# Performance work log

Measured on AMD Instinct MI355X. Metric: run time of the kernel, lower is better.

The kernel has to match this reference:

```python
import jax, jax.numpy as jnp
import numpy as np

# Model dims (from DecoderLSTM defaults)
H = 512       # hidden_size
E = 128       # embedding_dim == input_size
NC = 27       # num_class (output_size)
NE = 28       # num_embeddings = num_class + 1
B = 256       # batch
T = 512       # timesteps


def setup_inputs() -> dict:
    key = jax.random.key(0)
    ks = jax.random.split(key, 12)
    s = 0.05
    return {
        "target_inputs": jax.random.randint(ks[0], (B, T), 0, NE),
        "target_lengths": jax.random.randint(ks[1], (B,), 1, T + 1),
        "h0": jax.random.normal(ks[2], (4, B, H), dtype=jnp.float32),   # [num_layer*num_dirs, B, H]
        "c0": jax.random.normal(ks[3], (4, B, H), dtype=jnp.float32),
        "embed": jax.random.normal(ks[4], (NE, E), dtype=jnp.float32) * s,
        "Wih0": jax.random.normal(ks[5], (2, 4 * H, E), dtype=jnp.float32) * s,      # layer0 [dir,4H,E]
        "Wih1": jax.random.normal(ks[6], (2, 4 * H, 2 * H), dtype=jnp.float32) * s,  # layer1 [dir,4H,2H]
        "Whh": jax.random.normal(ks[7], (2, 2, 4 * H, H), dtype=jnp.float32) * s,    # [layer,dir,4H,H]
        "bih": jax.random.normal(ks[8], (2, 2, 4 * H), dtype=jnp.float32) * s,
        "bhh": jax.random.normal(ks[9], (2, 2, 4 * H), dtype=jnp.float32) * s,
        "Wout": jax.random.normal(ks[10], (NC, 2 * H), dtype=jnp.float32) * s,
        "bout": jax.random.normal(ks[11], (NC,), dtype=jnp.float32) * s,
    }


def _lstm_cell(x, h, c, Wih, Whh, b):
    # x: [B,in], h/c: [B,H]; PyTorch gate order i,f,g,o
    g = x @ Wih.T + h @ Whh.T + b
    i, f, gg, o = jnp.split(g, 4, axis=-1)
    c2 = jax.nn.sigmoid(f) * c + jax.nn.sigmoid(i) * jnp.tanh(gg)
    h2 = jax.nn.sigmoid(o) * jnp.tanh(c2)
    return h2, c2


def reference(target_inputs, target_lengths, h0, c0, embed,
              Wih0, Wih1, Whh, bih, bhh, Wout, bout):
    b = bih + bhh                              # [layer,dir,4H]
    x_emb = embed[target_inputs]               # [B,T,E]
    seq_len = target_inputs.shape[1]

    def step(carry, xt):
        h, c = carry                           # [4,B,H] each; layout layer*2+dir
        hf, cf = _lstm_cell(xt, h[0], c[0], Wih0[0], Whh[0, 0], b[0, 0])
        hb, cb = _lstm_cell(xt, h[1], c[1], Wih0[1], Whh[0, 1], b[0, 1])
        y0 = jnp.concatenate([hf, hb], axis=-1)                 # [B,2H]
        h2f, c2f = _lstm_cell(y0, h[2], c[2], Wih1[0], Whh[1, 0], b[1, 0])
        h2b, c2b = _lstm_cell(y0, h[3], c[3], Wih1[1], Whh[1, 1], b[1, 1])
        y1 = jnp.concatenate([h2f, h2b], axis=-1)               # [B,2H]
        hn = jnp.stack([hf, hb, h2f, h2b])
        cn = jnp.stack([cf, cb, c2f, c2b])
        return (hn, cn), y1 @ Wout.T + bout                      # logits [B,NC]

    _, logits_t = jax.lax.scan(step, (h0, c0), jnp.swapaxes(x_emb, 0, 1))
    logits = jnp.swapaxes(logits_t, 0, 1)                        # [B,T,NC]
    mask = jnp.arange(seq_len)[None, :] < target_lengths[:, None]
    outputs = jnp.where(mask[:, :, None], logits, jnp.zeros((), logits.dtype))
    return outputs, target_lengths
```

## Files before the change

kernel.cpp:

```cpp
#include <hip/hip_runtime.h>
#include <hip/hip_bf16.h>
#include <stdint.h>

typedef unsigned short ushort_t;
typedef unsigned char u8_t;
typedef unsigned long long u64_t;

#define H   512
#define E   128
#define NC  27
#define NE  28
#define B   256
#define T   512
#define FH  2048
#define NPH (T + 2)
#define NL0 64
#define NL1 128
#define NOUT 32
#define BHs (B * H)
#define WOFF_L0 131072
#define WOFF_L1 65536
#define LDS_BYTES (160 * 1024)
#define CROW 256

typedef __bf16 bf16x8 __attribute__((ext_vector_type(8)));
typedef float  f32x4  __attribute__((ext_vector_type(4)));

#define WAITV(n) asm volatile("s_waitcnt vmcnt(" #n ")" ::: "memory")
#define LADDER8(rem) do { if ((rem) >= 7) WAITV(7); else if ((rem) == 6) WAITV(6); \
                          else if ((rem) == 5) WAITV(5); else if ((rem) == 4) WAITV(4); \
                          else if ((rem) == 3) WAITV(3); else if ((rem) == 2) WAITV(2); \
                          else if ((rem) == 1) WAITV(1); else WAITV(0); } while (0)

__device__ __forceinline__ ushort_t f2b(float x) {
    uint32_t u = __float_as_uint(x);
    uint32_t r = (u + 0x7FFFu + ((u >> 16) & 1u)) >> 16;
    return (ushort_t)r;
}
__device__ __forceinline__ u8_t f2fp8(float x) {
    uint32_t u = __float_as_uint(x);
    uint32_t s = (u >> 24) & 0x80u;
    int E8 = (int)((u >> 23) & 0xffu);
    uint32_t M = u & 0x7fffffu;
    if (E8 == 0) return (u8_t)s;
    int e8 = E8 - 120;
    uint32_t code;
    if (e8 <= 0) {
        int sh = 1 - e8;
        if (sh > 23) return (u8_t)s;
        code = (0x800000u | M) >> sh;
    } else {
        code = ((uint32_t)e8 << 23) | M;
    }
    uint32_t r = (code + 0x7ffffu + ((code >> 20) & 1u)) >> 20;
    if (r > 0x7eu) r = 0x7eu;
    return (u8_t)(s | r);
}
__device__ __forceinline__ float sigm(float x) {
    return 1.f / (1.f + __expf(-x));
}
__device__ __forceinline__ void stc1(u8_t* p, u8_t v) {
    __hip_atomic_store(p, v, __ATOMIC_RELAXED, __HIP_MEMORY_SCOPE_AGENT);
}
__device__ __forceinline__ void stc2(ushort_t* p, ushort_t v) {
    __hip_atomic_store(p, v, __ATOMIC_RELAXED, __HIP_MEMORY_SCOPE_AGENT);
}
__device__ __forceinline__ void stc4f(float* p, float v) {
    __hip_atomic_store(p, v, __ATOMIC_RELAXED, __HIP_MEMORY_SCOPE_AGENT);
}
__device__ __forceinline__ bf16x8 ldc16(const ushort_t* p) {
    union { u64_t q[2]; bf16x8 v; } u;
    u.q[0] = __hip_atomic_load((const u64_t*)p,       __ATOMIC_RELAXED, __HIP_MEMORY_SCOPE_AGENT);
    u.q[1] = __hip_atomic_load(((const u64_t*)p) + 1, __ATOMIC_RELAXED, __HIP_MEMORY_SCOPE_AGENT);
    return u.v;
}
__device__ __forceinline__ void gload_lds16c(const void* g, void* l) {
    __builtin_amdgcn_global_load_lds(
        (const __attribute__((address_space(1))) void*)g,
        (__attribute__((address_space(3))) void*)l, 16, 0, 17);
}

__device__ __forceinline__ void stageA8(const u8_t* __restrict__ hsrc, int k0,
                                        char* chunk, int wave, int lane) {
    int gd = lane & 3;
    #pragma unroll
    for (int i = 0; i < 2; ++i) {
        int r = wave * 32 + i * 16 + (lane >> 2);
        int fr = (r & 3) ^ ((r >> 2) & 3);
        const u8_t* g = hsrc + (size_t)r * H + k0 + ((gd ^ fr) << 4);
        gload_lds16c((const void*)g, (void*)(chunk + wave * 2048 + i * 1024));
    }
}

__device__ __forceinline__ void stageB8(const u8_t* __restrict__ hsrc, int rb, int k0,
                                        char* chunk, int wave, int lane) {
    int r = wave * 16 + (lane >> 2);
    int gd = lane & 3;
    int fr = (r & 3) ^ ((r >> 2) & 3);
    const u8_t* g = hsrc + (size_t)(rb + r) * H + k0 + ((gd ^ fr) << 4);
    gload_lds16c((const void*)g, (void*)(chunk + wave * 1024));
}


__global__ void k_init(int* __restrict__ cnt) {
    for (int i = blockIdx.x * blockDim.x + threadIdx.x; i < 3 * NPH * CROW;
         i += gridDim.x * blockDim.x) cnt[i] = 0;
}

__global__ void k_g0(const float* __restrict__ embed, const float* __restrict__ Wih0,
                     const float* __restrict__ bih, const float* __restrict__ bhh,
                     float* __restrict__ G0, float* __restrict__ bias1) {
    int i = blockIdx.x * blockDim.x + threadIdx.x;
    if (i < 2 * NE * FH) {
        int d = i / (NE * FH);
        int rem = i % (NE * FH);
        int e = rem / FH;
        int n = rem % FH;
        int g = n >> 9, j = n & 511;
        const float* er = embed + (size_t)e * E;
        const float* wr = Wih0 + ((size_t)d * FH + n) * E;
        float s = 0.f;
        #pragma unroll 8
        for (int k = 0; k < E; ++k) s += er[k] * wr[k];
        G0[(((size_t)d * NE + e) * 512 + j) * 4 + g]
            = s + bih[(size_t)d * FH + n] + bhh[(size_t)d * FH + n];
    }
    if (i < 2 * FH) bias1[i] = bih[2 * FH + i] + bhh[2 * FH + i];
}

__global__ void k_state(const float* __restrict__ h0, ushort_t* __restrict__ hb16,
                        u8_t* __restrict__ hf8) {
    int i = blockIdx.x * blockDim.x + threadIdx.x;
    if (i >= 4 * B * H) return;
    int cell = i / (B * H);
    int rem  = i % (B * H);
    hb16[((size_t)(cell * 3 + 2)) * BHs + rem] = f2b(h0[i]);
    hf8 [((size_t)(cell * 3 + 2)) * BHs + rem] = f2fp8(h0[i]);
}

__global__ void k_tokT(const int* __restrict__ tok, int* __restrict__ tokT) {
    int i = blockIdx.x * blockDim.x + threadIdx.x;
    if (i < B * T) {
        int b = i / T, t = i % T;
        tokT[(size_t)t * B + b] = tok[i];
    }
}

__global__ void k_len(const int* __restrict__ lens, float* __restrict__ out_len) {
    int i = threadIdx.x;
    if (i < B) out_len[i] = (float)lens[i];
}

__device__ __forceinline__ int polled(const int* c) {
    int t = 0;
    #pragma unroll
    for (int i = 0; i < 16; ++i)
        t += __hip_atomic_load(c + i * 16, __ATOMIC_RELAXED, __HIP_MEMORY_SCOPE_AGENT);
    return t;
}

__device__ __forceinline__ void boundary(int* cntL0, int* cntL1, int* cntOUT,
                                         int role, int bid, int p) {
    __syncthreads();
    if (threadIdx.x == 0) {
        int* mine = (role == 0) ? cntL0 : (role == 1) ? cntL1 : cntOUT;
        __hip_atomic_fetch_add(mine + p * CROW + (bid & 15) * 16, 1,
                               __ATOMIC_RELAXED, __HIP_MEMORY_SCOPE_AGENT);
        const int q = p + 1;
        int nl0 = -1, nl1 = -1;
        if (role == 0) {
            if (q < T) {
                nl0 = q - 1;
                if (q >= 2) nl1 = q - 2;
            }
        } else if (role == 1) {
            if (q >= 1 && q <= T) nl0 = q - 1;
        } else {
            if (q >= 2) nl1 = q - 1;
        }
        for (;;) {
            int a = (nl0 >= 0) ? polled(cntL0 + nl0 * CROW) : NL0;
            int b = (nl1 >= 0) ? polled(cntL1 + nl1 * CROW) : NL1;
            if (a >= NL0 && b >= NL1) break;
            __builtin_amdgcn_s_sleep(2);
        }
    }
    __syncthreads();
    __builtin_amdgcn_sched_barrier(0);
}

__device__ __forceinline__ void gateL1(const int* cntL1, const int* cntOUT, int p) {
    __builtin_amdgcn_sched_barrier(0);
    if (threadIdx.x == 0) {
        for (;;) {
            int a = polled(cntL1 + (p - 1) * CROW);
            int b = (p >= 2) ? polled(cntOUT + (p - 2) * CROW) : NOUT;
            if (a >= NL1 && b >= NOUT) break;
            __builtin_amdgcn_s_sleep(2);
        }
    }
    __builtin_amdgcn_s_barrier();
    __builtin_amdgcn_sched_barrier(0);
}

__global__ __launch_bounds__(512, 2) void k_persist(
    const float* __restrict__ Whh, const float* __restrict__ Wih1,
    const float* __restrict__ G0, const float* __restrict__ bias1,
    const float* __restrict__ c0, ushort_t* __restrict__ hb16,
    u8_t* __restrict__ hf8,
    const int* __restrict__ tokT, const int* __restrict__ lens,
    const float* __restrict__ Wout, const float* __restrict__ bout,
    float* __restrict__ out, int* __restrict__ cnt)
{
    extern __shared__ char smem[];
    const int bid = blockIdx.x;
    const int tid = threadIdx.x;
    const int lane = tid & 63, wave = tid >> 6;
    const int lrow = lane & 15, kg = lane >> 4;
    const int row0 = wave * 32;
    const int sw8 = lrow & 7;

    int* cntL0  = cnt;
    int* cntL1  = cnt + NPH * CROW;
    int* cntOUT = cnt + 2 * NPH * CROW;
    const int role = (bid < NL0) ? 0 : (bid < NL0 + NL1) ? 1 : 2;

    int wksoff[2];
    #pragma unroll
    for (int ks = 0; ks < 2; ++ks)
        wksoff[ks] = (((ks * 4 + kg) ^ sw8) << 3);

    if (bid < 64) {
        const int cell = bid >> 5, jt = bid & 31, j0 = jt * 16;
        const float* Wsrc = Whh + (size_t)cell * FH * H;
        for (int r = wave; r < 64; r += 8) {
            int grow = (r >> 4) * 512 + j0 + (r & 15);
            const float* src = Wsrc + (size_t)grow * H;
            for (int c = lane; c < H; c += 64) {
                int slot = c >> 3;
                int ssw = (slot & ~7) | ((slot ^ r) & 7);
                *(u8_t*)(smem + WOFF_L0 + r * 512 + ssw * 8 + (c & 7)) = f2fp8(src[c]);
            }
        }
    } else if (bid < 192) {
        const int q = bid - 64;
        const int rem = q & 63, cell = 2 + (rem >> 5), jt = rem & 31, j0 = jt * 16;
        const float* Wi = Wih1 + (size_t)(cell - 2) * FH * (2 * H);
        const float* Wh = Whh + (size_t)cell * FH * H;
        for (int r = wave; r < 64; r += 8) {
            int grow = (r >> 4) * 512 + j0 + (r & 15);
            const float* si = Wi + (size_t)grow * (2 * H);
            const float* sh = Wh + (size_t)grow * H;
            for (int c = lane; c < 1536; c += 64) {
                float v = (c < 1024) ? si[c] : sh[c - 1024];
                int slot = c >> 3;
                int ssw = (slot & ~7) | ((slot ^ r) & 7);
                *(u8_t*)(smem + WOFF_L1 + r * 1536 + ssw * 8 + (c & 7)) = f2fp8(v);
            }
        }
    } else {
        for (int r = wave; r < NC; r += 8) {
            const float* src = Wout + (size_t)r * (2 * H);
            int sw = (r & 7) << 4;
            for (int c = lane; c < 2 * H; c += 64) {
                int byte = ((r * (2 * H) + c) * 2) ^ sw;
                *(ushort_t*)(smem + byte) = f2b(src[c]);
            }
        }
    }
    __syncthreads();

    if (bid < 64) {
        const int cell = bid >> 5, jt = bid & 31, j0 = jt * 16;
        const int j = j0 + lrow;
        const int fA = (lrow & 3) ^ ((lrow >> 2) & 3);
        int aoffK[2];
        #pragma unroll
        for (int ks = 0; ks < 2; ++ks)
            aoffK[ks] = (row0 + lrow) * 64 + ((((ks << 1) | (kg >> 1)) ^ fA) << 4) + ((kg & 1) << 3);
        int wgbase[4];
        #pragma unroll
        for (int g = 0; g < 4; ++g) wgbase[g] = WOFF_L0 + (g * 16 + lrow) * 512;

        float cv[8];
        #pragma unroll
        for (int i = 0; i < 8; ++i) {
            int bb = row0 + (i >> 2) * 16 + kg * 4 + (i & 3);
            cv[i] = c0[((size_t)cell * B + bb) * H + j];
        }
        f32x4 g0v[8];
        #pragma unroll
        for (int i = 0; i < 8; ++i) {
            int bb = row0 + (i >> 2) * 16 + kg * 4 + (i & 3);
            int tk = tokT[bb];
            g0v[i] = *(const f32x4*)(G0 + (((size_t)cell * NE + tk) * 512 + j) * 4);
        }

        for (int p = 0; p < NPH; ++p) {
            if (p < T) {
                const int pm3 = p % 3;
                const int parR = (pm3 + 2) % 3, parW = pm3;
                const u8_t* hsrc = hf8 + (size_t)(cell * 3 + parR) * BHs;

                #pragma unroll
                for (int c2 = 0; c2 < 8; ++c2)
                    stageA8(hsrc, c2 * 64, smem + c2 * 16384, wave, lane);

                f32x4 acc[2][4];
                #pragma unroll
                for (int m = 0; m < 2; ++m)
                    #pragma unroll
                    for (int g = 0; g < 4; ++g) acc[m][g] = (f32x4){0.f, 0.f, 0.f, 0.f};

                #pragma unroll
                for (int t = 0; t < 8; ++t) {
                    if (t == 0)      WAITV(14);
                    else if (t == 1) WAITV(12);
                    else if (t == 2) WAITV(10);
                    else if (t == 3) WAITV(8);
                    else if (t == 4) WAITV(6);
                    else if (t == 5) WAITV(4);
                    else if (t == 6) WAITV(2);
                    else             WAITV(0);
                    __builtin_amdgcn_sched_barrier(0);
                    const char* Ab = smem + t * 16384;
                    u64_t aA[2][2], wW[2][4];
                    #pragma unroll
                    for (int ks = 0; ks < 2; ++ks) {
                        aA[ks][0] = *(const u64_t*)(Ab + aoffK[ks]);
                        aA[ks][1] = *(const u64_t*)(Ab + aoffK[ks] + 1024);
                        #pragma unroll
                        for (int g = 0; g < 4; ++g)
                            wW[ks][g] = *(const u64_t*)(smem + wgbase[g] + t * 64 + wksoff[ks]);
                    }
                    asm volatile("s_waitcnt lgkmcnt(0)" ::: "memory");
                    __builtin_amdgcn_sched_barrier(0);
                    #pragma unroll
                    for (int ks = 0; ks < 2; ++ks)
                        #pragma unroll
                        for (int g = 0; g < 4; ++g) {
                            acc[0][g] = __builtin_amdgcn_mfma_f32_16x16x32_fp8_fp8(
                                (long)aA[ks][0], (long)wW[ks][g], acc[0][g], 0, 0, 0);
                            acc[1][g] = __builtin_amdgcn_mfma_f32_16x16x32_fp8_fp8(
                                (long)aA[ks][1], (long)wW[ks][g], acc[1][g], 0, 0, 0);
                        }
                }

                #pragma unroll
                for (int i = 0; i < 8; ++i) {
                    int mf = i >> 2, r = i & 3;
                    int bb = row0 + mf * 16 + kg * 4 + r;
                    float gi = acc[mf][0][r] + g0v[i][0];
                    float gf = acc[mf][1][r] + g0v[i][1];
                    float gg = acc[mf][2][r] + g0v[i][2];
                    float go = acc[mf][3][r] + g0v[i][3];
                    float ii = sigm(gi), ff = sigm(gf), oo = sigm(go);
                    float tg = tanhf(gg);
                    float cn = ff * cv[i] + ii * tg;
                    cv[i] = cn;
                    float hn = oo * tanhf(cn);
                    stc1(&hf8[((size_t)(cell * 3 + parW) * B + bb) * H + j], f2fp8(hn));
                }
                if (p + 1 < T) {
                    #pragma unroll
                    for (int i = 0; i < 8; ++i) {
                        int bb = row0 + (i >> 2) * 16 + kg * 4 + (i & 3);
                        int tk = tokT[(size_t)(p + 1) * B + bb];
                        g0v[i] = *(const f32x4*)(G0 + (((size_t)cell * NE + tk) * 512 + j) * 4);
                    }
                }
            }
            if (p < NPH - 1) boundary(cntL0, cntL1, cntOUT, role, bid, p);
        }
    } else if (bid < 192) {
        const int q = bid - 64;
        const int bt = q >> 6, rem = q & 63;
        const int cell = 2 + (rem >> 5), jt = rem & 31;
        const int j0 = jt * 16, rb = bt * 128;
        const int j = j0 + lrow;
        const int fB = (lrow & 3) ^ ((wave * 4 + (lrow >> 2)) & 3);
        int aoffB[2];
        #pragma unroll
        for (int ks = 0; ks < 2; ++ks)
            aoffB[ks] = (wave * 16 + lrow) * 64 + ((((ks << 1) | (kg >> 1)) ^ fB) << 4) + ((kg & 1) << 3);
        int wgbase[4];
        #pragma unroll
        for (int g = 0; g < 4; ++g) wgbase[g] = WOFF_L1 + (g * 16 + lrow) * 1536;

        float b1v[4];
        #pragma unroll
        for (int g = 0; g < 4; ++g) b1v[g] = bias1[(size_t)(cell - 2) * FH + g * 512 + j];

        float cv[4];
        #pragma unroll
        for (int r = 0; r < 4; ++r) {
            int bb = rb + wave * 16 + kg * 4 + r;
            cv[r] = c0[((size_t)cell * B + bb) * H + j];
        }

        for (int p = 0; p < NPH; ++p) {
            if (p >= 1 && p <= T) {
                const int pm3 = p % 3;
                const int parY  = (pm3 + 2) % 3;
                const int parR2 = (pm3 + 1) % 3;
                const int parW  = parY;
                const u8_t* base0 = hf8 + (size_t)(0 * 3 + parY) * BHs;
                const u8_t* base1 = hf8 + (size_t)(1 * 3 + parY) * BHs;
                const u8_t* base2 = hf8 + (size_t)(cell * 3 + parR2) * BHs;

                f32x4 acc[4];
                #pragma unroll
                for (int g = 0; g < 4; ++g) acc[g] = (f32x4){0.f, 0.f, 0.f, 0.f};

                #pragma unroll
                for (int c2 = 0; c2 < 8; ++c2)
                    stageB8(base0, rb, c2 * 64, smem + c2 * 8192, wave, lane);

                #pragma unroll
                for (int t = 0; t < 16; ++t) {
                    LADDER8(15 - t);
                    __builtin_amdgcn_sched_barrier(0);
                    const char* Ab = smem + (t & 7) * 8192;
                    u64_t aA[2], wW[2][4];
                    #pragma unroll
                    for (int ks = 0; ks < 2; ++ks) {
                        aA[ks] = *(const u64_t*)(Ab + aoffB[ks]);
                        #pragma unroll
                        for (int g = 0; g < 4; ++g)
                            wW[ks][g] = *(const u64_t*)(smem + wgbase[g] + t * 64 + wksoff[ks]);
                    }
                    asm volatile("s_waitcnt lgkmcnt(0)" ::: "memory");
                    __builtin_amdgcn_sched_barrier(0);
                    if (t < 8)
                        stageB8(base1, rb, t * 64, smem + (t & 7) * 8192, wave, lane);
                    __builtin_amdgcn_sched_barrier(0);
                    #pragma unroll
                    for (int ks = 0; ks < 2; ++ks)
                        #pragma unroll
                        for (int g = 0; g < 4; ++g)
                            acc[g] = __builtin_amdgcn_mfma_f32_16x16x32_fp8_fp8(
                                (long)aA[ks], (long)wW[ks][g], acc[g], 0, 0, 0);
                }

                gateL1(cntL1, cntOUT, p);

                #pragma unroll
                for (int c2 = 0; c2 < 8; ++c2)
                    stageB8(base2, rb, c2 * 64, smem + c2 * 8192, wave, lane);

                #pragma unroll
                for (int tt = 0; tt < 8; ++tt) {
                    const int t = 16 + tt;
                    LADDER8(7 - tt);
                    __builtin_amdgcn_sched_barrier(0);
                    const char* Ab = smem + (tt & 7) * 8192;
                    u64_t aA[2], wW[2][4];
                    #pragma unroll
                    for (int ks = 0; ks < 2; ++ks) {
                        aA[ks] = *(const u64_t*)(Ab + aoffB[ks]);
                        #pragma unroll
                        for (int g = 0; g < 4; ++g)
                            wW[ks][g] = *(const u64_t*)(smem + wgbase[g] + t * 64 + wksoff[ks]);
                    }
                    asm volatile("s_waitcnt lgkmcnt(0)" ::: "memory");
                    __builtin_amdgcn_sched_barrier(0);
                    #pragma unroll
                    for (int ks = 0; ks < 2; ++ks)
                        #pragma unroll
                        for (int g = 0; g < 4; ++g)
                            acc[g] = __builtin_amdgcn_mfma_f32_16x16x32_fp8_fp8(
                                (long)aA[ks], (long)wW[ks][g], acc[g], 0, 0, 0);
                }

                #pragma unroll
                for (int r = 0; r < 4; ++r) {
                    int bb = rb + wave * 16 + kg * 4 + r;
                    float gi = acc[0][r] + b1v[0];
                    float gf = acc[1][r] + b1v[1];
                    float gg = acc[2][r] + b1v[2];
                    float go = acc[3][r] + b1v[3];
                    float ii = sigm(gi), ff = sigm(gf), oo = sigm(go);
                    float tg = tanhf(gg);
                    float cn = ff * cv[r] + ii * tg;
                    cv[r] = cn;
                    float hn = oo * tanhf(cn);
                    size_t hi = ((size_t)(cell * 3 + parW) * B + bb) * H + j;
                    stc1(&hf8[hi], f2fp8(hn));
                    stc2(&hb16[hi], f2b(hn));
                }
            }
            if (p < NPH - 1) boundary(cntL0, cntL1, cntOUT, role, bid, p);
        }
    } else {
        const int b = (bid - 192) * 8 + wave;
        const int c = lane & 31, kh = lane >> 5;
        const int half = lane >> 5, qq = lane & 31;
        const int sww = (c & 7) << 4;
        const int rowbase = c * 2048;
        const int lenb = lens[b];
        const float bo = (c < NC) ? bout[c] : 0.f;
        char* scr = smem + 57344 + wave * 2048;

        for (int p = 0; p < NPH; ++p) {
            if (p >= 2) {
                const int t2 = p - 2;
                const int parL = (p % 3 + 1) % 3;
                {
                    const ushort_t* src = hb16 + (size_t)((2 + half) * 3 + parL) * BHs
                                        + (size_t)b * H + qq * 16;
                    bf16x8 v0 = ldc16(src);
                    bf16x8 v1 = ldc16(src + 8);
                    char* dst = scr + half * 1024 + qq * 32;
                    *(bf16x8*)dst = v0;
                    *(bf16x8*)(dst + 16) = v1;
                }
                __syncthreads();
                float sum = 0.f;
                if (c < NC) {
                    const char* ybase = scr + kh * 1024;
                    #pragma unroll 8
                    for (int t = 0; t < 64; ++t) {
                        bf16x8 v = *(const bf16x8*)(ybase + t * 16);
                        bf16x8 w = *(const bf16x8*)(smem + rowbase + ((kh * 1024 + t * 16) ^ sww));
                        #pragma unroll
                        for (int i = 0; i < 8; ++i) sum += (float)v[i] * (float)w[i];
                    }
                }
                sum += __shfl_xor(sum, 32);
                if (kh == 0 && c < NC) {
                    float val = (t2 < lenb) ? (sum + bo) : 0.f;
                    stc4f(&out[((size_t)b * T + t2) * NC + c], val);
                }
            }
            if (p < NPH - 1) boundary(cntL0, cntL1, cntOUT, role, bid, p);
        }
    }
}


extern "C" void kernel_launch(void* const* d_in, const int* in_sizes, int n_in,
                              void* d_out, int out_size, void* d_ws, size_t ws_size,
                              hipStream_t stream) {
    const int*   tok   = (const int*)d_in[0];
    const int*   lens  = (const int*)d_in[1];
    const float* h0    = (const float*)d_in[2];
    const float* c0    = (const float*)d_in[3];
    const float* embed = (const float*)d_in[4];
    const float* Wih0  = (const float*)d_in[5];
    const float* Wih1  = (const float*)d_in[6];
    const float* Whh   = (const float*)d_in[7];
    const float* bih   = (const float*)d_in[8];
    const float* bhh   = (const float*)d_in[9];
    const float* Wout  = (const float*)d_in[10];
    const float* bout  = (const float*)d_in[11];
    float* out = (float*)d_out;

    ushort_t* hb16  = (ushort_t*)d_ws;
    u8_t*     hf8   = (u8_t*)(hb16 + (size_t)4 * 3 * B * H);
    float*    G0    = (float*)(hf8 + (size_t)4 * 3 * B * H);
    float*    bias1 = G0 + 2 * NE * FH;
    int*      cnt   = (int*)(bias1 + 2 * FH);
    int*      tokT  = cnt + 3 * NPH * CROW;

    (void)hipFuncSetAttribute((const void*)k_persist,
                              hipFuncAttributeMaxDynamicSharedMemorySize, LDS_BYTES);

    k_init<<<256, 256, 0, stream>>>(cnt);
    k_g0<<<(2 * NE * FH + 255) / 256, 256, 0, stream>>>(embed, Wih0, bih, bhh, G0, bias1);
    k_state<<<(4 * B * H + 255) / 256, 256, 0, stream>>>(h0, hb16, hf8);
    k_tokT<<<(B * T + 255) / 256, 256, 0, stream>>>(tok, tokT);
    k_len<<<1, 256, 0, stream>>>(lens, out + (size_t)B * T * NC);

    k_persist<<<NL0 + NL1 + NOUT, 512, LDS_BYTES, stream>>>(
        Whh, Wih1, G0, bias1, c0, hb16, hf8, tokT, lens, Wout, bout, out, cnt);
}
```

Baseline: 4.697 ms.

## Retile layer-0 blocks to 128 batch rows by 32 hidden units

```diff
diff --git a/kernel.cpp b/kernel.cpp
--- a/kernel.cpp
+++ b/kernel.cpp
@@ -18,8 +18,7 @@
 #define NL1 128
 #define NOUT 32
 #define BHs (B * H)
-#define WOFF_L0 131072
-#define WOFF_L1 65536
+#define WOFF 65536
 #define LDS_BYTES (160 * 1024)
 #define CROW 256
 
@@ -78,18 +77,6 @@
     __builtin_amdgcn_global_load_lds(
         (const __attribute__((address_space(1))) void*)g,
         (__attribute__((address_space(3))) void*)l, 16, 0, 17);
-}
-
-__device__ __forceinline__ void stageA8(const u8_t* __restrict__ hsrc, int k0,
-                                        char* chunk, int wave, int lane) {
-    int gd = lane & 3;
-    #pragma unroll
-    for (int i = 0; i < 2; ++i) {
-        int r = wave * 32 + i * 16 + (lane >> 2);
-        int fr = (r & 3) ^ ((r >> 2) & 3);
-        const u8_t* g = hsrc + (size_t)r * H + k0 + ((gd ^ fr) << 4);
-        gload_lds16c((const void*)g, (void*)(chunk + wave * 2048 + i * 1024));
-    }
 }
 
 __device__ __forceinline__ void stageB8(const u8_t* __restrict__ hsrc, int rb, int k0,
@@ -217,7 +204,6 @@
     const int tid = threadIdx.x;
     const int lane = tid & 63, wave = tid >> 6;
     const int lrow = lane & 15, kg = lane >> 4;
-    const int row0 = wave * 32;
     const int sw8 = lrow & 7;
 
     int* cntL0  = cnt;
@@ -229,17 +215,22 @@
     #pragma unroll
     for (int ks = 0; ks < 2; ++ks)
         wksoff[ks] = (((ks * 4 + kg) ^ sw8) << 3);
+    const int fB = (lrow & 3) ^ ((wave * 4 + (lrow >> 2)) & 3);
+    int aoffB[2];
+    #pragma unroll
+    for (int ks = 0; ks < 2; ++ks)
+        aoffB[ks] = (wave * 16 + lrow) * 64 + ((((ks << 1) | (kg >> 1)) ^ fB) << 4) + ((kg & 1) << 3);
 
     if (bid < 64) {
-        const int cell = bid >> 5, jt = bid & 31, j0 = jt * 16;
+        const int cell = bid >> 5, rem0 = bid & 31, jt = rem0 & 15, j0 = jt * 32;
         const float* Wsrc = Whh + (size_t)cell * FH * H;
-        for (int r = wave; r < 64; r += 8) {
-            int grow = (r >> 4) * 512 + j0 + (r & 15);
+        for (int r = wave; r < 128; r += 8) {
+            int grow = (r >> 5) * 512 + j0 + (r & 31);
             const float* src = Wsrc + (size_t)grow * H;
             for (int c = lane; c < H; c += 64) {
                 int slot = c >> 3;
                 int ssw = (slot & ~7) | ((slot ^ r) & 7);
-                *(u8_t*)(smem + WOFF_L0 + r * 512 + ssw * 8 + (c & 7)) = f2fp8(src[c]);
+                *(u8_t*)(smem + WOFF + r * 512 + ssw * 8 + (c & 7)) = f2fp8(src[c]);
             }
         }
     } else if (bid < 192) {
@@ -255,7 +246,7 @@
                 float v = (c < 1024) ? si[c] : sh[c - 1024];
                 int slot = c >> 3;
                 int ssw = (slot & ~7) | ((slot ^ r) & 7);
-                *(u8_t*)(smem + WOFF_L1 + r * 1536 + ssw * 8 + (c & 7)) = f2fp8(v);
+                *(u8_t*)(smem + WOFF + r * 1536 + ssw * 8 + (c & 7)) = f2fp8(v);
             }
         }
     } else {
@@ -271,30 +262,35 @@
     __syncthreads();
 
     if (bid < 64) {
-        const int cell = bid >> 5, jt = bid & 31, j0 = jt * 16;
-        const int j = j0 + lrow;
-        const int fA = (lrow & 3) ^ ((lrow >> 2) & 3);
-        int aoffK[2];
+        const int cell = bid >> 5, rem0 = bid & 31;
+        const int bt = rem0 >> 4, jt = rem0 & 15;
+        const int j0 = jt * 32, rb = bt * 128;
+        int wgbase[4][2];
         #pragma unroll
-        for (int ks = 0; ks < 2; ++ks)
-            aoffK[ks] = (row0 + lrow) * 64 + ((((ks << 1) | (kg >> 1)) ^ fA) << 4) + ((kg & 1) << 3);
-        int wgbase[4];
-        #pragma unroll
-        for (int g = 0; g < 4; ++g) wgbase[g] = WOFF_L0 + (g * 16 + lrow) * 512;
+        for (int g = 0; g < 4; ++g)
+            #pragma unroll
+            for (int jf = 0; jf < 2; ++jf)
+                wgbase[g][jf] = WOFF + (g * 32 + jf * 16 + lrow) * 512;
 
         float cv[8];
         #pragma unroll
-        for (int i = 0; i < 8; ++i) {
-            int bb = row0 + (i >> 2) * 16 + kg * 4 + (i & 3);
-            cv[i] = c0[((size_t)cell * B + bb) * H + j];
-        }
+        for (int jf = 0; jf < 2; ++jf)
+            #pragma unroll
+            for (int r = 0; r < 4; ++r) {
+                int bb = rb + wave * 16 + kg * 4 + r;
+                int j2 = j0 + jf * 16 + lrow;
+                cv[jf * 4 + r] = c0[((size_t)cell * B + bb) * H + j2];
+            }
         f32x4 g0v[8];
         #pragma unroll
-        for (int i = 0; i < 8; ++i) {
-            int bb = row0 + (i >> 2) * 16 + kg * 4 + (i & 3);
-            int tk = tokT[bb];
-            g0v[i] = *(const f32x4*)(G0 + (((size_t)cell * NE + tk) * 512 + j) * 4);
-        }
+        for (int jf = 0; jf < 2; ++jf)
+            #pragma unroll
+            for (int r = 0; r < 4; ++r) {
+                int bb = rb + wave * 16 + kg * 4 + r;
+                int tk = tokT[bb];
+                int j2 = j0 + jf * 16 + lrow;
+                g0v[jf * 4 + r] = *(const f32x4*)(G0 + (((size_t)cell * NE + tk) * 512 + j2) * 4);
+            }
 
         for (int p = 0; p < NPH; ++p) {
             if (p < T) {
@@ -304,70 +300,71 @@
 
                 #pragma unroll
                 for (int c2 = 0; c2 < 8; ++c2)
-                    stageA8(hsrc, c2 * 64, smem + c2 * 16384, wave, lane);
-
-                f32x4 acc[2][4];
-                #pragma unroll
-                for (int m = 0; m < 2; ++m)
-                    #pragma unroll
-                    for (int g = 0; g < 4; ++g) acc[m][g] = (f32x4){0.f, 0.f, 0.f, 0.f};
+                    stageB8(hsrc, rb, c2 * 64, smem + c2 * 8192, wave, lane);
+
+                f32x4 acc[4][2];
+                #pragma unroll
+                for (int g = 0; g < 4; ++g)
+                    #pragma unroll
+                    for (int jf = 0; jf < 2; ++jf) acc[g][jf] = (f32x4){0.f, 0.f, 0.f, 0.f};
 
                 #pragma unroll
                 for (int t = 0; t < 8; ++t) {
-                    if (t == 0)      WAITV(14);
-                    else if (t == 1) WAITV(12);
-                    else if (t == 2) WAITV(10);
-                    else if (t == 3) WAITV(8);
-                    else if (t == 4) WAITV(6);
-                    else if (t == 5) WAITV(4);
-                    else if (t == 6) WAITV(2);
-                    else             WAITV(0);
-                    __builtin_amdgcn_sched_barrier(0);
-                    const char* Ab = smem + t * 16384;
-                    u64_t aA[2][2], wW[2][4];
+                    LADDER8(7 - t);
+                    __builtin_amdgcn_sched_barrier(0);
+                    const char* Ab = smem + t * 8192;
+                    u64_t aA[2], wW[2][4][2];
                     #pragma unroll
                     for (int ks = 0; ks < 2; ++ks) {
-                        aA[ks][0] = *(const u64_t*)(Ab + aoffK[ks]);
-                        aA[ks][1] = *(const u64_t*)(Ab + aoffK[ks] + 1024);
+                        aA[ks] = *(const u64_t*)(Ab + aoffB[ks]);
                         #pragma unroll
                         for (int g = 0; g < 4; ++g)
-                            wW[ks][g] = *(const u64_t*)(smem + wgbase[g] + t * 64 + wksoff[ks]);
+                            #pragma unroll
+                            for (int jf = 0; jf < 2; ++jf)
+                                wW[ks][g][jf] = *(const u64_t*)(smem + wgbase[g][jf] + t * 64 + wksoff[ks]);
                     }
                     asm volatile("s_waitcnt lgkmcnt(0)" ::: "memory");
                     __builtin_amdgcn_sched_barrier(0);
                     #pragma unroll
                     for (int ks = 0; ks < 2; ++ks)
                         #pragma unroll
-                        for (int g = 0; g < 4; ++g) {
-                            acc[0][g] = __builtin_amdgcn_mfma_f32_16x16x32_fp8_fp8(
-                                (long)aA[ks][0], (long)wW[ks][g], acc[0][g], 0, 0, 0);
-                            acc[1][g] = __builtin_amdgcn_mfma_f32_16x16x32_fp8_fp8(
-                                (long)aA[ks][1], (long)wW[ks][g], acc[1][g], 0, 0, 0);
+                        for (int g = 0; g < 4; ++g)
+                            #pragma unroll
+                            for (int jf = 0; jf < 2; ++jf)
+                                acc[g][jf] = __builtin_amdgcn_mfma_f32_16x16x32_fp8_fp8(
+                                    (long)aA[ks], (long)wW[ks][g][jf], acc[g][jf], 0, 0, 0);
+                }
+
+                #pragma unroll
+                for (int jf = 0; jf < 2; ++jf) {
+                    int j2 = j0 + jf * 16 + lrow;
+                    #pragma unroll
+                    for (int r = 0; r < 4; ++r) {
+                        int bb = rb + wave * 16 + kg * 4 + r;
+                        f32x4 gq = g0v[jf * 4 + r];
+                        float gi = acc[0][jf][r] + gq[0];
+                        float gf = acc[1][jf][r] + gq[1];
+                        float gg = acc[2][jf][r] + gq[2];
+                        float go = acc[3][jf][r] + gq[3];
+                        float ii = sigm(gi), ff = sigm(gf), oo = sigm(go);
+                        float tg = tanhf(gg);
+                        int ci = jf * 4 + r;
+                        float cn = ff * cv[ci] + ii * tg;
+                        cv[ci] = cn;
+                        float hn = oo * tanhf(cn);
+                        stc1(&hf8[((size_t)(cell * 3 + parW) * B + bb) * H + j2], f2fp8(hn));
+                    }
+                }
+                if (p + 1 < T) {
+                    #pragma unroll
+                    for (int jf = 0; jf < 2; ++jf)
+                        #pragma unroll
+                        for (int r = 0; r < 4; ++r) {
+                            int bb = rb + wave * 16 + kg * 4 + r;
+                            int tk = tokT[(size_t)(p + 1) * B + bb];
+                            int j2 = j0 + jf * 16 + lrow;
+                            g0v[jf * 4 + r] = *(const f32x4*)(G0 + (((size_t)cell * NE + tk) * 512 + j2) * 4);
                         }
-                }
-
-                #pragma unroll
-                for (int i = 0; i < 8; ++i) {
-                    int mf = i >> 2, r = i & 3;
-                    int bb = row0 + mf * 16 + kg * 4 + r;
-                    float gi = acc[mf][0][r] + g0v[i][0];
-                    float gf = acc[mf][1][r] + g0v[i][1];
-                    float gg = acc[mf][2][r] + g0v[i][2];
-                    float go = acc[mf][3][r] + g0v[i][3];
-                    float ii = sigm(gi), ff = sigm(gf), oo = sigm(go);
-                    float tg = tanhf(gg);
-                    float cn = ff * cv[i] + ii * tg;
-                    cv[i] = cn;
-                    float hn = oo * tanhf(cn);
-                    stc1(&hf8[((size_t)(cell * 3 + parW) * B + bb) * H + j], f2fp8(hn));
-                }
-                if (p + 1 < T) {
-                    #pragma unroll
-                    for (int i = 0; i < 8; ++i) {
-                        int bb = row0 + (i >> 2) * 16 + kg * 4 + (i & 3);
-                        int tk = tokT[(size_t)(p + 1) * B + bb];
-                        g0v[i] = *(const f32x4*)(G0 + (((size_t)cell * NE + tk) * 512 + j) * 4);
-                    }
                 }
             }
             if (p < NPH - 1) boundary(cntL0, cntL1, cntOUT, role, bid, p);
@@ -378,14 +375,9 @@
         const int cell = 2 + (rem >> 5), jt = rem & 31;
         const int j0 = jt * 16, rb = bt * 128;
         const int j = j0 + lrow;
-        const int fB = (lrow & 3) ^ ((wave * 4 + (lrow >> 2)) & 3);
-        int aoffB[2];
-        #pragma unroll
-        for (int ks = 0; ks < 2; ++ks)
-            aoffB[ks] = (wave * 16 + lrow) * 64 + ((((ks << 1) | (kg >> 1)) ^ fB) << 4) + ((kg & 1) << 3);
         int wgbase[4];
         #pragma unroll
-        for (int g = 0; g < 4; ++g) wgbase[g] = WOFF_L1 + (g * 16 + lrow) * 1536;
+        for (int g = 0; g < 4; ++g) wgbase[g] = WOFF + (g * 16 + lrow) * 1536;
 
         float b1v[4];
         #pragma unroll
```

Result: slower. 4.819 ms (+2.6%).
